# Optimization experiments

Hardware: AMD Instinct MI355X
Metric: run time of the kernel (lower is better)

Reference implementation:

```python
import jax, jax.numpy as jnp
import numpy as np

B, C, L = 8, 256, 2048


def setup_inputs() -> dict:
    key = jax.random.key(0)
    ks = jax.random.split(key, 7)
    s = 0.05
    return {
        "x": jax.random.normal(ks[0], (B, C, L), dtype=jnp.float32),
        "Wq": jax.random.normal(ks[1], (C, C), dtype=jnp.float32) * s,
        "bq": jax.random.normal(ks[2], (C,), dtype=jnp.float32) * s,
        "Wk": jax.random.normal(ks[3], (C, C), dtype=jnp.float32) * s,
        "bk": jax.random.normal(ks[4], (C,), dtype=jnp.float32) * s,
        "Wv": jax.random.normal(ks[5], (C, C), dtype=jnp.float32) * s,
        "bv": jax.random.normal(ks[6], (C,), dtype=jnp.float32) * s,
    }


def reference(x, Wq, bq, Wk, bk, Wv, bv):
    # Conv1d with kernel_size=1 == per-position linear over channels.
    # x: [B, C, L]
    scale = x.shape[1] ** (-0.5)
    q = jnp.einsum('oc,bcl->bol', Wq, x) + bq[None, :, None]  # [B,C,L]
    k = jnp.einsum('oc,bcl->bol', Wk, x) + bk[None, :, None]
    v = jnp.einsum('oc,bcl->bol', Wv, x) + bv[None, :, None]
    scores = jnp.einsum('bcl,bcm->blm', q, k) * scale          # [B,L,L]
    attn = jax.nn.softmax(scores, axis=-1)
    context = jnp.einsum('blm,bcm->bcl', attn, v)              # [B,C,L]
    return context + x
```

## Files before the change

kernel.cpp:

```cpp
#include <hip/hip_runtime.h>

#define NB 8
#define NC 256
#define NL 2048
#define SCALE 0.0625f

typedef __attribute__((ext_vector_type(8))) __bf16 bf16x8;
typedef __attribute__((ext_vector_type(4))) float f32x4;
typedef __attribute__((ext_vector_type(4))) unsigned int u32x4;
typedef __attribute__((ext_vector_type(4))) unsigned short u16x4;
typedef __attribute__((ext_vector_type(8))) unsigned short u16x8;

static __device__ __forceinline__ unsigned short f2b(float f) {
    unsigned int u = __builtin_bit_cast(unsigned int, f);
    u += 0x7fffu + ((u >> 16) & 1u);
    return (unsigned short)(u >> 16);
}

__global__ void wconv_kernel(const float* __restrict__ Wq,
                             const float* __restrict__ Wk,
                             const float* __restrict__ Wv,
                             unsigned short* __restrict__ Wbf)
{
    const int base = (blockIdx.x * 256 + threadIdx.x) * 4;
    const int mat  = base >> 16;
    const int off  = base & 65535;
    const float* W = (mat == 0) ? Wq : (mat == 1) ? Wk : Wv;
    float4 w = *(const float4*)&W[off];
    u16x4 p = {f2b(w.x), f2b(w.y), f2b(w.z), f2b(w.w)};
    *(u16x4*)&Wbf[base] = p;
}

__global__ __launch_bounds__(256, 2) void xprep_kernel(
    const float* __restrict__ x, unsigned short* __restrict__ xT)
{
    const int b  = blockIdx.z;
    const int c0 = blockIdx.y * 64;
    const int l0 = blockIdx.x * 64;
    const int t  = threadIdx.x;

    __shared__ unsigned short Tr[64][68];

    #pragma unroll
    for (int p = 0; p < 4; ++p) {
        const int c  = p * 16 + (t >> 4);
        const int lg = t & 15;
        float4 xv = *(const float4*)&x[((size_t)(b * NC + c0 + c)) * NL + l0 + lg * 4];
        u16x4 pk = {f2b(xv.x), f2b(xv.y), f2b(xv.z), f2b(xv.w)};
        *(u16x4*)&Tr[c][lg * 4] = pk;
    }
    __syncthreads();
    #pragma unroll
    for (int j = 0; j < 2; ++j) {
        const int chunk = t + 256 * j;
        const int l  = chunk >> 3;
        const int ck = chunk & 7;
        u16x8 o;
        #pragma unroll
        for (int i = 0; i < 8; ++i) o[i] = Tr[ck * 8 + i][l];
        *(u16x8*)&xT[((size_t)(b * NL + l0 + l)) * NC + c0 + ck * 8] = o;
    }
}

__global__ __launch_bounds__(256, 2) void qkv_mfma(
    const unsigned short* __restrict__ xT,
    const unsigned short* __restrict__ Wbf,
    const float* __restrict__ bq, const float* __restrict__ bk,
    const float* __restrict__ bv,
    unsigned short* __restrict__ qT, unsigned short* __restrict__ kT,
    unsigned short* __restrict__ vo)
{
    const int raw = blockIdx.x;
    const int b   = raw & 7;
    const int rem = raw >> 3;
    const int mat = rem >> 5;
    const int lt0 = (rem & 31) * 64;
    const int t    = threadIdx.x;
    const int w    = t >> 6;
    const int lane = t & 63;
    const int ln15 = lane & 15;
    const int quad = lane >> 4;

    __shared__ __align__(16) unsigned short XT[64 * 256];
    __shared__ __align__(16) unsigned short WC[256 * 64];

    const unsigned short* Wm = Wbf + mat * 65536;
    const float* bias = (mat == 0) ? bq : (mat == 1) ? bk : bv;

    float bvals[4][4];
    #pragma unroll
    for (int ot = 0; ot < 4; ++ot)
        #pragma unroll
        for (int r = 0; r < 4; ++r)
            bvals[ot][r] = bias[w * 64 + ot * 16 + quad * 4 + r];

    #pragma unroll
    for (int s = 0; s < 8; ++s) {
        const int il = w * 8 + s;
        const int n  = il * 2 + (lane >> 5);
        const int p  = lane & 31;
        const int g  = p ^ (n & 15);
        const unsigned short* gp = &xT[((size_t)(b * NL + lt0 + n)) * NC + g * 8];
        __builtin_amdgcn_global_load_lds(
            (const __attribute__((address_space(1))) unsigned int*)gp,
            (__attribute__((address_space(3))) unsigned int*)&XT[il * 512],
            16, 0, 0);
    }

    f32x4 acc[4][4];
    #pragma unroll
    for (int i = 0; i < 4; ++i)
        #pragma unroll
        for (int j = 0; j < 4; ++j) acc[i][j] = f32x4{0.f, 0.f, 0.f, 0.f};

    for (int k0 = 0; k0 < 4; ++k0) {
        if (k0) __syncthreads();
        #pragma unroll
        for (int s = 0; s < 8; ++s) {
            const int il = w * 8 + s;
            const int o  = il * 8 + (lane >> 3);
            const int p  = lane & 7;
            const int g  = p ^ (o & 7);
            const unsigned short* gp = &Wm[(size_t)o * NC + k0 * 64 + g * 8];
            __builtin_amdgcn_global_load_lds(
                (const __attribute__((address_space(1))) unsigned int*)gp,
                (__attribute__((address_space(3))) unsigned int*)&WC[il * 512],
                16, 0, 0);
        }
        __syncthreads();

        #pragma unroll
        for (int ks = 0; ks < 2; ++ks) {
            bf16x8 xf[4];
            #pragma unroll
            for (int lt = 0; lt < 4; ++lt) {
                const int l  = lt * 16 + ln15;
                const int kc = k0 * 8 + ks * 4 + quad;
                const int pp = kc ^ (l & 15);
                xf[lt] = __builtin_bit_cast(bf16x8, *(const u32x4*)&XT[l * 256 + pp * 8]);
            }
            #pragma unroll
            for (int ot = 0; ot < 4; ++ot) {
                const int o  = w * 64 + ot * 16 + ln15;
                const int pp = (ks * 4 + quad) ^ (o & 7);
                bf16x8 wf = __builtin_bit_cast(bf16x8, *(const u32x4*)&WC[o * 64 + pp * 8]);
                #pragma unroll
                for (int lt = 0; lt < 4; ++lt)
                    acc[ot][lt] = __builtin_amdgcn_mfma_f32_16x16x32_bf16(
                                      wf, xf[lt], acc[ot][lt], 0, 0, 0);
            }
        }
    }

    if (mat < 2) {
        unsigned short* out = (mat == 0) ? qT : kT;
        #pragma unroll
        for (int ot = 0; ot < 4; ++ot) {
            const int o_base = w * 64 + ot * 16 + quad * 4;
            #pragma unroll
            for (int lt = 0; lt < 4; ++lt) {
                const int l = lt0 + lt * 16 + ln15;
                u16x4 pk;
                #pragma unroll
                for (int r = 0; r < 4; ++r)
                    pk[r] = f2b(acc[ot][lt][r] + bvals[ot][r]);
                *(u16x4*)&out[((size_t)(b * NL + l)) * NC + o_base] = pk;
            }
        }
    } else {
        #pragma unroll
        for (int ot = 0; ot < 4; ++ot)
            #pragma unroll
            for (int lt = 0; lt < 4; ++lt) {
                const int l = lt0 + lt * 16 + ln15;
                #pragma unroll
                for (int r = 0; r < 4; ++r) {
                    const int o = w * 64 + ot * 16 + quad * 4 + r;
                    vo[((size_t)(b * NC + o)) * NL + l] = f2b(acc[ot][lt][r] + bvals[ot][r]);
                }
            }
    }
}

__global__ __launch_bounds__(512, 1) void attn_kernel(
    const unsigned short* __restrict__ qT,
    const unsigned short* __restrict__ kT,
    const unsigned short* __restrict__ v,
    const float* __restrict__ x,
    float* __restrict__ out)
{
    const int raw  = blockIdx.x;
    const int b    = raw & 7;
    const int l0   = (raw >> 3) * 64;
    const int t    = threadIdx.x;
    const int w    = t >> 6;
    const int lane = t & 63;
    const int ln15 = lane & 15;
    const int quad = lane >> 4;
    const int qg   = w & 3;
    const int kg   = w >> 2;

    __shared__ __align__(16) char smem[139776];
    unsigned short* Kb0 = (unsigned short*)smem;
    unsigned short* Kb1 = (unsigned short*)(smem + 32768);
    unsigned short* Vb0 = (unsigned short*)(smem + 65536);
    unsigned short* Vb1 = (unsigned short*)(smem + 98304);
    unsigned short* Plds = (unsigned short*)(smem + 131072);
    float* denomP = (float*)(smem + 139264);
    float (*ctxbuf)[68] = (float(*)[68])smem;

    bf16x8 qf[8];
    {
        const size_t qrow = ((size_t)b * NL + l0 + qg * 16 + ln15) * NC;
        #pragma unroll
        for (int kt = 0; kt < 8; ++kt)
            qf[kt] = __builtin_bit_cast(bf16x8,
                        *(const u32x4*)&qT[qrow + kt * 32 + quad * 8]);
    }

    f32x4 ctx[16];
    #pragma unroll
    for (int i = 0; i < 16; ++i) ctx[i] = f32x4{0.f, 0.f, 0.f, 0.f};
    float dacc[4] = {0.f, 0.f, 0.f, 0.f};

    auto stage = [&](int mt, unsigned short* Kd, unsigned short* Vd) {
        const int m0 = mt * 64;
        #pragma unroll
        for (int s = 0; s < 4; ++s) {
            const int il = w * 4 + s;
            const int n  = il * 2 + (lane >> 5);
            const int g  = (lane & 31) ^ (n & 15);
            const unsigned short* gp = &kT[((size_t)b * NL + m0 + n) * NC + g * 8];
            __builtin_amdgcn_global_load_lds(
                (const __attribute__((address_space(1))) unsigned int*)gp,
                (__attribute__((address_space(3))) unsigned int*)&Kd[il * 512],
                16, 0, 0);
        }
        #pragma unroll
        for (int s = 0; s < 4; ++s) {
            const int il = w * 4 + s;
            const int c  = il * 8 + (lane >> 3);
            const int g  = (lane & 7) ^ (c & 7);
            const unsigned short* gp = &v[((size_t)(b * NC + c)) * NL + m0 + g * 8];
            __builtin_amdgcn_global_load_lds(
                (const __attribute__((address_space(1))) unsigned int*)gp,
                (__attribute__((address_space(3))) unsigned int*)&Vd[il * 512],
                16, 0, 0);
        }
    };

    stage(0, Kb0, Vb0);
    __syncthreads();

    for (int mt = 0; mt < 32; ++mt) {
        if (mt < 31) {
            if (mt & 1) stage(mt + 1, Kb0, Vb0);
            else        stage(mt + 1, Kb1, Vb1);
        }
        const unsigned short* Kd = (mt & 1) ? Kb1 : Kb0;
        const unsigned short* Vd = (mt & 1) ? Vb1 : Vb0;

        f32x4 sacc[2];
        sacc[0] = f32x4{0.f, 0.f, 0.f, 0.f};
        sacc[1] = f32x4{0.f, 0.f, 0.f, 0.f};
        #pragma unroll
        for (int nt = 0; nt < 2; ++nt) {
            const int n = kg * 32 + nt * 16 + ln15;
            #pragma unroll
            for (int kt = 0; kt < 8; ++kt) {
                const int p = (kt * 4 + quad) ^ ln15;
                bf16x8 bf = __builtin_bit_cast(bf16x8,
                              *(const u32x4*)&Kd[n * 256 + p * 8]);
                sacc[nt] = __builtin_amdgcn_mfma_f32_16x16x32_bf16(
                               qf[kt], bf, sacc[nt], 0, 0, 0);
            }
        }

        float rs[4] = {0.f, 0.f, 0.f, 0.f};
        #pragma unroll
        for (int nt = 0; nt < 2; ++nt) {
            #pragma unroll
            for (int r = 0; r < 4; ++r) {
                float e = __expf(sacc[nt][r] * SCALE);
                rs[r] += e;
                const int ip = qg * 16 + quad * 4 + r;
                const int j  = kg * 32 + nt * 16 + ln15;
                const int pc = (j >> 3) ^ (ip & 7);
                Plds[ip * 64 + pc * 8 + (j & 7)] = f2b(e);
            }
        }
        #pragma unroll
        for (int r = 0; r < 4; ++r) {
            rs[r] += __shfl_xor(rs[r], 1, 64);
            rs[r] += __shfl_xor(rs[r], 2, 64);
            rs[r] += __shfl_xor(rs[r], 4, 64);
            rs[r] += __shfl_xor(rs[r], 8, 64);
            dacc[r] += rs[r];
        }

        bf16x8 pf;
        {
            const int m = qg * 16 + ln15;
            const int p = (kg * 4 + quad) ^ (m & 7);
            pf = __builtin_bit_cast(bf16x8, *(const u32x4*)&Plds[m * 64 + p * 8]);
        }
        #pragma unroll
        for (int ct = 0; ct < 16; ++ct) {
            const int c = ct * 16 + ln15;
            const int p = (kg * 4 + quad) ^ (c & 7);
            bf16x8 vb = __builtin_bit_cast(bf16x8,
                          *(const u32x4*)&Vd[c * 64 + p * 8]);
            ctx[ct] = __builtin_amdgcn_mfma_f32_16x16x32_bf16(
                          pf, vb, ctx[ct], 0, 0, 0);
        }

        __syncthreads();
    }

    if (kg == 1) {
        #pragma unroll
        for (int ct = 0; ct < 16; ++ct) {
            const int c = ct * 16 + ln15;
            #pragma unroll
            for (int r = 0; r < 4; ++r)
                ctxbuf[c][qg * 16 + quad * 4 + r] = ctx[ct][r];
        }
    }
    if (ln15 == 0) {
        #pragma unroll
        for (int r = 0; r < 4; ++r)
            denomP[kg * 64 + qg * 16 + quad * 4 + r] = dacc[r];
    }
    __syncthreads();
    if (kg == 0) {
        float rinv[4];
        #pragma unroll
        for (int r = 0; r < 4; ++r) {
            const int ql = qg * 16 + quad * 4 + r;
            rinv[r] = 1.0f / (denomP[ql] + denomP[64 + ql]);
        }
        #pragma unroll
        for (int ct = 0; ct < 16; ++ct) {
            const int c = ct * 16 + ln15;
            #pragma unroll
            for (int r = 0; r < 4; ++r) {
                const int ql = qg * 16 + quad * 4 + r;
                ctxbuf[c][ql] = (ctx[ct][r] + ctxbuf[c][ql]) * rinv[r];
            }
        }
    }
    __syncthreads();

    #pragma unroll
    for (int p = 0; p < 8; ++p) {
        const int f  = t + 512 * p;
        const int c  = f >> 4;
        const int lg = (f & 15) * 4;
        const size_t idx = ((size_t)(b * NC + c)) * NL + l0 + lg;
        float4 xv = *(const float4*)&x[idx];
        float4 cv = *(const float4*)&ctxbuf[c][lg];
        float4 o = make_float4(cv.x + xv.x, cv.y + xv.y, cv.z + xv.z, cv.w + xv.w);
        *(float4*)&out[idx] = o;
    }
}

extern "C" void kernel_launch(void* const* d_in, const int* in_sizes, int n_in,
                              void* d_out, int out_size, void* d_ws, size_t ws_size,
                              hipStream_t stream) {
    const float* x  = (const float*)d_in[0];
    const float* Wq = (const float*)d_in[1];
    const float* bq = (const float*)d_in[2];
    const float* Wk = (const float*)d_in[3];
    const float* bk = (const float*)d_in[4];
    const float* Wv = (const float*)d_in[5];
    const float* bv = (const float*)d_in[6];
    float* out = (float*)d_out;

    const size_t plane = (size_t)NB * NC * NL;
    unsigned short* qT  = (unsigned short*)d_ws;
    unsigned short* kT  = qT + plane;
    unsigned short* v   = kT + plane;
    unsigned short* xT  = v + plane;
    unsigned short* Wbf = xT + plane;

    wconv_kernel<<<192, 256, 0, stream>>>(Wq, Wk, Wv, Wbf);

    dim3 gx(NL / 64, NC / 64, NB);
    xprep_kernel<<<gx, 256, 0, stream>>>(x, xT);

    qkv_mfma<<<768, 256, 0, stream>>>(xT, Wbf, bq, bk, bv, qT, kT, v);

    attn_kernel<<<256, 512, 0, stream>>>(qT, kT, v, x, out);
}
```

Measured before the change: 165.3 us.

## Fuse x transpose/convert into QKV projection and prepack weights in MFMA fragment order

Drops the separate xprep kernel and the bf16 xT round trip through global memory. The fused QKV kernel loads fp32 x directly, converts it to bf16 and writes it transposed with a swizzle into LDS. Each block computes all three projections for one 64-position tile, keeping x fragments in registers across them. The weight conversion now prepacks weights in MFMA fragment layout, so the kernel reads weight fragments straight from global memory without staging them in LDS. The trade-off is heavy register use and scattered 2-byte LDS stores during the transpose.

```diff
diff --git a/kernel.cpp b/kernel.cpp
--- a/kernel.cpp
+++ b/kernel.cpp
@@ -22,48 +22,23 @@
                              const float* __restrict__ Wv,
                              unsigned short* __restrict__ Wbf)
 {
-    const int base = (blockIdx.x * 256 + threadIdx.x) * 4;
-    const int mat  = base >> 16;
-    const int off  = base & 65535;
+    const int fid  = blockIdx.x * 4 + (threadIdx.x >> 6);
+    const int lane = threadIdx.x & 63;
+    const int mat  = fid >> 7;
+    const int oT   = (fid >> 3) & 15;
+    const int kt   = fid & 7;
     const float* W = (mat == 0) ? Wq : (mat == 1) ? Wk : Wv;
-    float4 w = *(const float4*)&W[off];
-    u16x4 p = {f2b(w.x), f2b(w.y), f2b(w.z), f2b(w.w)};
-    *(u16x4*)&Wbf[base] = p;
-}
-
-__global__ __launch_bounds__(256, 2) void xprep_kernel(
-    const float* __restrict__ x, unsigned short* __restrict__ xT)
-{
-    const int b  = blockIdx.z;
-    const int c0 = blockIdx.y * 64;
-    const int l0 = blockIdx.x * 64;
-    const int t  = threadIdx.x;
-
-    __shared__ unsigned short Tr[64][68];
-
-    #pragma unroll
-    for (int p = 0; p < 4; ++p) {
-        const int c  = p * 16 + (t >> 4);
-        const int lg = t & 15;
-        float4 xv = *(const float4*)&x[((size_t)(b * NC + c0 + c)) * NL + l0 + lg * 4];
-        u16x4 pk = {f2b(xv.x), f2b(xv.y), f2b(xv.z), f2b(xv.w)};
-        *(u16x4*)&Tr[c][lg * 4] = pk;
-    }
-    __syncthreads();
-    #pragma unroll
-    for (int j = 0; j < 2; ++j) {
-        const int chunk = t + 256 * j;
-        const int l  = chunk >> 3;
-        const int ck = chunk & 7;
-        u16x8 o;
-        #pragma unroll
-        for (int i = 0; i < 8; ++i) o[i] = Tr[ck * 8 + i][l];
-        *(u16x8*)&xT[((size_t)(b * NL + l0 + l)) * NC + c0 + ck * 8] = o;
-    }
-}
-
-__global__ __launch_bounds__(256, 2) void qkv_mfma(
-    const unsigned short* __restrict__ xT,
+    const int o = oT * 16 + (lane & 15);
+    const int c = kt * 32 + (lane >> 4) * 8;
+    float4 a  = *(const float4*)&W[(size_t)o * NC + c];
+    float4 b2 = *(const float4*)&W[(size_t)o * NC + c + 4];
+    u16x8 p = {f2b(a.x), f2b(a.y), f2b(a.z), f2b(a.w),
+               f2b(b2.x), f2b(b2.y), f2b(b2.z), f2b(b2.w)};
+    *(u16x8*)&Wbf[(size_t)fid * 512 + lane * 8] = p;
+}
+
+__global__ __launch_bounds__(512, 2) void qkv_fused(
+    const float* __restrict__ x,
     const unsigned short* __restrict__ Wbf,
     const float* __restrict__ bq, const float* __restrict__ bk,
     const float* __restrict__ bv,
@@ -72,9 +47,7 @@
 {
     const int raw = blockIdx.x;
     const int b   = raw & 7;
-    const int rem = raw >> 3;
-    const int mat = rem >> 5;
-    const int lt0 = (rem & 31) * 64;
+    const int lt0 = (raw >> 3) * 64;
     const int t    = threadIdx.x;
     const int w    = t >> 6;
     const int lane = t & 63;
@@ -82,103 +55,94 @@
     const int quad = lane >> 4;
 
     __shared__ __align__(16) unsigned short XT[64 * 256];
-    __shared__ __align__(16) unsigned short WC[256 * 64];
-
-    const unsigned short* Wm = Wbf + mat * 65536;
-    const float* bias = (mat == 0) ? bq : (mat == 1) ? bk : bv;
-
-    float bvals[4][4];
+
+    {
+        const int c  = t >> 1;
+        const int hh = t & 1;
+        const float* xr = &x[((size_t)(b * NC + c)) * NL + lt0 + hh * 32];
+        const int cc = c >> 3, c7 = c & 7;
+        #pragma unroll
+        for (int j = 0; j < 8; ++j) {
+            float4 xv = *(const float4*)&xr[j * 4];
+            const int lb = hh * 32 + j * 4;
+            unsigned short e0 = f2b(xv.x), e1 = f2b(xv.y),
+                           e2 = f2b(xv.z), e3 = f2b(xv.w);
+            XT[(lb + 0) * 256 + (cc ^ ((lb + 0) & 15)) * 8 + c7] = e0;
+            XT[(lb + 1) * 256 + (cc ^ ((lb + 1) & 15)) * 8 + c7] = e1;
+            XT[(lb + 2) * 256 + (cc ^ ((lb + 2) & 15)) * 8 + c7] = e2;
+            XT[(lb + 3) * 256 + (cc ^ ((lb + 3) & 15)) * 8 + c7] = e3;
+        }
+    }
+    __syncthreads();
+
+    bf16x8 xf[4][8];
     #pragma unroll
-    for (int ot = 0; ot < 4; ++ot)
-        #pragma unroll
-        for (int r = 0; r < 4; ++r)
-            bvals[ot][r] = bias[w * 64 + ot * 16 + quad * 4 + r];
+    for (int lt = 0; lt < 4; ++lt) {
+        const int l = lt * 16 + ln15;
+        #pragma unroll
+        for (int kt = 0; kt < 8; ++kt) {
+            const int kc = kt * 4 + quad;
+            const int pos = kc ^ (l & 15);
+            xf[lt][kt] = __builtin_bit_cast(bf16x8, *(const u32x4*)&XT[l * 256 + pos * 8]);
+        }
+    }
 
     #pragma unroll
-    for (int s = 0; s < 8; ++s) {
-        const int il = w * 8 + s;
-        const int n  = il * 2 + (lane >> 5);
-        const int p  = lane & 31;
-        const int g  = p ^ (n & 15);
-        const unsigned short* gp = &xT[((size_t)(b * NL + lt0 + n)) * NC + g * 8];
-        __builtin_amdgcn_global_load_lds(
-            (const __attribute__((address_space(1))) unsigned int*)gp,
-            (__attribute__((address_space(3))) unsigned int*)&XT[il * 512],
-            16, 0, 0);
-    }
-
-    f32x4 acc[4][4];
-    #pragma unroll
-    for (int i = 0; i < 4; ++i)
-        #pragma unroll
-        for (int j = 0; j < 4; ++j) acc[i][j] = f32x4{0.f, 0.f, 0.f, 0.f};
-
-    for (int k0 = 0; k0 < 4; ++k0) {
-        if (k0) __syncthreads();
-        #pragma unroll
-        for (int s = 0; s < 8; ++s) {
-            const int il = w * 8 + s;
-            const int o  = il * 8 + (lane >> 3);
-            const int p  = lane & 7;
-            const int g  = p ^ (o & 7);
-            const unsigned short* gp = &Wm[(size_t)o * NC + k0 * 64 + g * 8];
-            __builtin_amdgcn_global_load_lds(
-                (const __attribute__((address_space(1))) unsigned int*)gp,
-                (__attribute__((address_space(3))) unsigned int*)&WC[il * 512],
-                16, 0, 0);
-        }
-        __syncthreads();
-
-        #pragma unroll
-        for (int ks = 0; ks < 2; ++ks) {
-            bf16x8 xf[4];
+    for (int mat = 0; mat < 3; ++mat) {
+        const float* bias = (mat == 0) ? bq : (mat == 1) ? bk : bv;
+        float bvals[2][4];
+        #pragma unroll
+        for (int ot = 0; ot < 2; ++ot)
+            #pragma unroll
+            for (int r = 0; r < 4; ++r)
+                bvals[ot][r] = bias[w * 32 + ot * 16 + quad * 4 + r];
+
+        f32x4 acc[2][4];
+        #pragma unroll
+        for (int i = 0; i < 2; ++i)
+            #pragma unroll
+            for (int j = 0; j < 4; ++j) acc[i][j] = f32x4{0.f, 0.f, 0.f, 0.f};
+
+        const size_t wb = ((size_t)(mat * 16 + w * 2) * 8) * 512 + lane * 8;
+        #pragma unroll
+        for (int kt = 0; kt < 8; ++kt) {
+            bf16x8 wf0 = __builtin_bit_cast(bf16x8, *(const u32x4*)&Wbf[wb + (size_t)kt * 512]);
+            bf16x8 wf1 = __builtin_bit_cast(bf16x8, *(const u32x4*)&Wbf[wb + (size_t)(8 + kt) * 512]);
             #pragma unroll
             for (int lt = 0; lt < 4; ++lt) {
-                const int l  = lt * 16 + ln15;
-                const int kc = k0 * 8 + ks * 4 + quad;
-                const int pp = kc ^ (l & 15);
-                xf[lt] = __builtin_bit_cast(bf16x8, *(const u32x4*)&XT[l * 256 + pp * 8]);
-            }
-            #pragma unroll
-            for (int ot = 0; ot < 4; ++ot) {
-                const int o  = w * 64 + ot * 16 + ln15;
-                const int pp = (ks * 4 + quad) ^ (o & 7);
-                bf16x8 wf = __builtin_bit_cast(bf16x8, *(const u32x4*)&WC[o * 64 + pp * 8]);
+                acc[0][lt] = __builtin_amdgcn_mfma_f32_16x16x32_bf16(wf0, xf[lt][kt], acc[0][lt], 0, 0, 0);
+                acc[1][lt] = __builtin_amdgcn_mfma_f32_16x16x32_bf16(wf1, xf[lt][kt], acc[1][lt], 0, 0, 0);
+            }
+        }
+
+        if (mat < 2) {
+            unsigned short* out = (mat == 0) ? qT : kT;
+            #pragma unroll
+            for (int ot = 0; ot < 2; ++ot) {
+                const int o_base = w * 32 + ot * 16 + quad * 4;
                 #pragma unroll
-                for (int lt = 0; lt < 4; ++lt)
-                    acc[ot][lt] = __builtin_amdgcn_mfma_f32_16x16x32_bf16(
-                                      wf, xf[lt], acc[ot][lt], 0, 0, 0);
-            }
-        }
-    }
-
-    if (mat < 2) {
-        unsigned short* out = (mat == 0) ? qT : kT;
-        #pragma unroll
-        for (int ot = 0; ot < 4; ++ot) {
-            const int o_base = w * 64 + ot * 16 + quad * 4;
-            #pragma unroll
-            for (int lt = 0; lt < 4; ++lt) {
-                const int l = lt0 + lt * 16 + ln15;
-                u16x4 pk;
+                for (int lt = 0; lt < 4; ++lt) {
+                    const int l = lt0 + lt * 16 + ln15;
+                    u16x4 pk;
+                    #pragma unroll
+                    for (int r = 0; r < 4; ++r)
+                        pk[r] = f2b(acc[ot][lt][r] + bvals[ot][r]);
+                    *(u16x4*)&out[((size_t)(b * NL + l)) * NC + o_base] = pk;
+                }
+            }
+        } else {
+            #pragma unroll
+            for (int ot = 0; ot < 2; ++ot)
                 #pragma unroll
-                for (int r = 0; r < 4; ++r)
-                    pk[r] = f2b(acc[ot][lt][r] + bvals[ot][r]);
-                *(u16x4*)&out[((size_t)(b * NL + l)) * NC + o_base] = pk;
-            }
-        }
-    } else {
-        #pragma unroll
-        for (int ot = 0; ot < 4; ++ot)
-            #pragma unroll
-            for (int lt = 0; lt < 4; ++lt) {
-                const int l = lt0 + lt * 16 + ln15;
-                #pragma unroll
-                for (int r = 0; r < 4; ++r) {
-                    const int o = w * 64 + ot * 16 + quad * 4 + r;
-                    vo[((size_t)(b * NC + o)) * NL + l] = f2b(acc[ot][lt][r] + bvals[ot][r]);
+                for (int lt = 0; lt < 4; ++lt) {
+                    const int l = lt0 + lt * 16 + ln15;
+                    #pragma unroll
+                    for (int r = 0; r < 4; ++r) {
+                        const int o = w * 32 + ot * 16 + quad * 4 + r;
+                        vo[((size_t)(b * NC + o)) * NL + l] = f2b(acc[ot][lt][r] + bvals[ot][r]);
+                    }
                 }
-            }
+        }
     }
 }
 
@@ -380,15 +344,11 @@
     unsigned short* qT  = (unsigned short*)d_ws;
     unsigned short* kT  = qT + plane;
     unsigned short* v   = kT + plane;
-    unsigned short* xT  = v + plane;
-    unsigned short* Wbf = xT + plane;
-
-    wconv_kernel<<<192, 256, 0, stream>>>(Wq, Wk, Wv, Wbf);
-
-    dim3 gx(NL / 64, NC / 64, NB);
-    xprep_kernel<<<gx, 256, 0, stream>>>(x, xT);
-
-    qkv_mfma<<<768, 256, 0, stream>>>(xT, Wbf, bq, bk, bv, qT, kT, v);
+    unsigned short* Wbf = v + plane;
+
+    wconv_kernel<<<96, 256, 0, stream>>>(Wq, Wk, Wv, Wbf);
+
+    qkv_fused<<<256, 512, 0, stream>>>(x, Wbf, bq, bk, bv, qT, kT, v);
 
     attn_kernel<<<256, 512, 0, stream>>>(qT, kT, v, x, out);
 }
```

New measurement: 166.4 us. Within noise of the previous version (+0.6%).
